# Optimization experiments

Hardware: AMD Instinct MI355X
Metric: run time of the kernel (lower is better)

The kernel has to match this reference:

```python
import jax, jax.numpy as jnp
import numpy as np
import math

B, N, DIM = 4, 4096, 1024
HEADS, DHEAD, NRF = 16, 64, 64
STAB = 1e-6  # numerical_stabilizer


def setup_inputs() -> dict:
    key = jax.random.key(0)
    k1, k2, k3, k4 = jax.random.split(key, 4)
    x = jax.random.normal(k1, (B, N, DIM), dtype=jnp.float32)
    W_qkv = jax.random.normal(k2, (DIM, 3 * HEADS * DHEAD), dtype=jnp.float32) * (1.0 / math.sqrt(DIM))
    RF = jax.random.normal(k3, (HEADS, DHEAD, NRF), dtype=jnp.float32) / math.sqrt(NRF)
    W_out = jax.random.normal(k4, (HEADS * DHEAD, DIM), dtype=jnp.float32) * (1.0 / math.sqrt(HEADS * DHEAD))
    b_out = jnp.zeros((DIM,), dtype=jnp.float32)
    return {"x": x, "W_qkv": W_qkv, "RF": RF, "W_out": W_out, "b_out": b_out}


def _phi(t, RF):
    # kernel transformation: project onto random features, then ReLU (default kernel)
    return jax.nn.relu(jnp.einsum('bhnd,hdr->bhnr', t, RF))


def reference(x, W_qkv, RF, W_out, b_out):
    b, n, _ = x.shape
    qkv = x @ W_qkv                                  # [b, n, 3*h*d]
    q, k, v = jnp.split(qkv, 3, axis=-1)
    def to_heads(t):
        return t.reshape(b, n, HEADS, DHEAD).transpose(0, 2, 1, 3)  # [b,h,n,d]
    q, k, v = to_heads(q), to_heads(k), to_heads(v)

    phi_q = _phi(q, RF)                              # [b,h,n,r]
    phi_k = _phi(k, RF)                              # [b,h,n,r]

    # linear-complexity FAVOR+ attention
    kv = jnp.einsum('bhnr,bhnd->bhrd', phi_k, v)     # [b,h,r,d]
    out = jnp.einsum('bhnr,bhrd->bhnd', phi_q, kv)   # [b,h,n,d]
    # normalizer: einsum('bhnr,bhmr->bhn') == phi_q @ sum_m(phi_k)
    k_sum = phi_k.sum(axis=2)                        # [b,h,r]
    normalizer = jnp.einsum('bhnr,bhr->bhn', phi_q, k_sum)[..., None] + STAB
    out = out / normalizer

    out = out.transpose(0, 2, 1, 3).reshape(b, n, HEADS * DHEAD)
    out = out @ W_out + b_out
    return out
```

## Files before the change

### kernel.cpp

```cpp
#include <hip/hip_runtime.h>


typedef __attribute__((ext_vector_type(8))) short s8v;
typedef __attribute__((ext_vector_type(4))) short s4v;
typedef __attribute__((ext_vector_type(4))) float f4v;
typedef __attribute__((ext_vector_type(4))) int   i4v;

#define MFMA16(a, b, c) __builtin_amdgcn_mfma_f32_16x16x32_bf16((a), (b), (c), 0, 0, 0)

__device__ __forceinline__ unsigned short f2bf(float f) {
  unsigned int u = __builtin_bit_cast(unsigned int, f);
  unsigned int r = (u + 0x7FFFu + ((u >> 16) & 1u)) >> 16;
  return (unsigned short)r;
}

__device__ __forceinline__ int swz(int p) {
  return p ^ (((p >> 7) & 7) << 4);
}

__device__ __forceinline__ void gl_lds16(const void* g, void* l) {
  __builtin_amdgcn_global_load_lds(
      (const __attribute__((address_space(1))) void*)g,
      (__attribute__((address_space(3))) void*)l, 16, 0, 0);
}

__global__ __launch_bounds__(256) void cvt_bf16(const float* __restrict__ in,
                                                unsigned short* __restrict__ out,
                                                int n4) {
  int i = blockIdx.x * 256 + threadIdx.x;
  if (i >= n4) return;
  f4v v = ((const f4v*)in)[i];
  s4v o;
#pragma unroll
  for (int j = 0; j < 4; ++j) o[j] = (short)f2bf(v[j]);
  ((s4v*)out)[i] = o;
}

__global__ __launch_bounds__(256) void transpose_cvt(const float* __restrict__ in,
                                                     unsigned short* __restrict__ out,
                                                     int R, int C) {
  __shared__ float tile[32][33];
  const int tx = threadIdx.x, ty = threadIdx.y;
  const int z = blockIdx.z;
  const float* inz = in + (size_t)z * R * C;
  unsigned short* outz = out + (size_t)z * R * C;
  const int c0 = blockIdx.x * 32, r0 = blockIdx.y * 32;
#pragma unroll
  for (int j = 0; j < 4; ++j)
    tile[ty + j * 8][tx] = inz[(size_t)(r0 + ty + j * 8) * C + c0 + tx];
  __syncthreads();
#pragma unroll
  for (int j = 0; j < 4; ++j)
    outz[(size_t)(c0 + ty + j * 8) * R + r0 + tx] = f2bf(tile[tx][ty + j * 8]);
}

template <int MODE>
__global__ __launch_bounds__(512, 2) void gemm256(const unsigned short* __restrict__ A,
                                                  const unsigned short* __restrict__ Bt,
                                                  void* __restrict__ Cout,
                                                  const float* __restrict__ bias,
                                                  int Nn, int K, int NTN, int CPX) {
  __shared__ __align__(128) unsigned short smem[65536];
  const int t = threadIdx.x, w = t >> 6, lane = t & 63;
  const int wm = w >> 2, wn = w & 3;
  const int fr = lane & 15, c16 = (lane >> 4) * 16;
  const int nkt = K >> 6;

  const int bid = blockIdx.x;
  const int wg = (bid & 7) * CPX + (bid >> 3);
  const int tm = wg / NTN, tn = wg % NTN;

  const unsigned short* gA = A + (size_t)tm * 256 * K;
  const unsigned short* gB = Bt + (size_t)tn * 256 * K;

  const int s0 = swz(t * 16);
  const int s1 = swz(8192 + t * 16);
  const int goff0 = (s0 >> 7) * K + ((s0 & 127) >> 1);
  const int goff1 = ((s1 - 8192) >> 7) * K + ((s1 & 127) >> 1) + 64 * K;
  const int woff = w * 1024;

  auto stage = [&](int T2, int part) {
    if (T2 >= nkt) return;
    char* reg = (char*)smem + (((T2 & 1) * 4 + part) << 14);
    const unsigned short* gp =
        (part < 2 ? gA : gB) + (size_t)((part & 1) * 128) * K + T2 * 64;
    gl_lds16(gp + goff0, reg + woff);
    gl_lds16(gp + goff1, reg + 8192 + woff);
  };

  f4v acc[8][4] = {};

  stage(0, 0); stage(0, 1); stage(0, 2); stage(0, 3);

  auto rdA = [&](int mh, s8v (&a)[4][2], const char* Ar) {
#pragma unroll
    for (int i = 0; i < 4; ++i)
#pragma unroll
      for (int ks = 0; ks < 2; ++ks) {
        int p = swz((mh * 64 + i * 16 + fr) * 128 + ks * 64 + c16);
        a[i][ks] = *(const s8v*)(Ar + p);
      }
  };
  auto rdB = [&](int nh, s8v (&b)[2][2], const char* Br, int brow) {
#pragma unroll
    for (int j = 0; j < 2; ++j)
#pragma unroll
      for (int ks = 0; ks < 2; ++ks) {
        int p = swz((brow + nh * 32 + j * 16 + fr) * 128 + ks * 64 + c16);
        b[j][ks] = *(const s8v*)(Br + p);
      }
  };
  auto mmac = [&](int mh, int nh, const s8v (&a)[4][2], const s8v (&b)[2][2]) {
    __builtin_amdgcn_s_setprio(1);
#pragma unroll
    for (int i = 0; i < 4; ++i)
#pragma unroll
      for (int j = 0; j < 2; ++j) {
        acc[mh * 4 + i][nh * 2 + j] = MFMA16(a[i][0], b[j][0], acc[mh * 4 + i][nh * 2 + j]);
        acc[mh * 4 + i][nh * 2 + j] = MFMA16(a[i][1], b[j][1], acc[mh * 4 + i][nh * 2 + j]);
      }
    __builtin_amdgcn_s_setprio(0);
  };

  const int brow = (wn & 1) * 64;
  for (int T = 0; T < nkt; ++T) {
    const int d = T & 1;
    const char* Ar = (const char*)smem + ((d * 4 + wm) << 14);
    const char* Br = (const char*)smem + ((d * 4 + 2 + (wn >> 1)) << 14);
    asm volatile("s_waitcnt vmcnt(0)" ::: "memory");
    __builtin_amdgcn_s_barrier();
    __builtin_amdgcn_sched_barrier(0);
    stage(T + 1, 0); stage(T + 1, 1); stage(T + 1, 2); stage(T + 1, 3);
    s8v a[4][2], b0[2][2], b1[2][2];
    rdA(0, a, Ar); rdB(0, b0, Br, brow); rdB(1, b1, Br, brow);
    mmac(0, 0, a, b0);
    mmac(0, 1, a, b1);
    rdA(1, a, Ar);
    mmac(1, 1, a, b1);
    mmac(1, 0, a, b0);
  }

#pragma unroll
  for (int m = 0; m < 8; ++m)
#pragma unroll
    for (int n = 0; n < 4; ++n) {
      const int row = tm * 256 + wm * 128 + m * 16 + (lane >> 4) * 4;
      const int col = tn * 256 + wn * 64 + n * 16 + fr;
      if (MODE == 0) {
        unsigned short* C = (unsigned short*)Cout;
#pragma unroll
        for (int r = 0; r < 4; ++r)
          C[(size_t)(row + r) * Nn + col] = f2bf(acc[m][n][r]);
      } else {
        float* C = (float*)Cout;
        const float bv = bias[col];
#pragma unroll
        for (int r = 0; r < 4; ++r)
          C[(size_t)(row + r) * Nn + col] = acc[m][n][r] + bv;
      }
    }
}

__global__ __launch_bounds__(256) void phik_kv(const unsigned short* __restrict__ qkv,
                                               const unsigned short* __restrict__ RFt,
                                               float* __restrict__ kvpart) {
  __shared__ unsigned short RFl[2 * 64 * 32];
  __shared__ unsigned short Kl[2 * 128 * 32];
  __shared__ unsigned short pht[64 * 136];
  __shared__ unsigned short vt[80 * 136];
  const int t = threadIdx.x, w = t >> 6, lane = t & 63;
  const int och = blockIdx.x, h = blockIdx.y, b = blockIdx.z;
  const int fr = lane & 15, kg = (lane >> 4) * 8;

#pragma unroll
  for (int i = 0; i < 2; ++i) {
    int unit = i * 256 + w * 64 + lane;
    int p = unit >> 8, rem = unit & 255;
    int r = rem >> 2, cg = (rem & 3) * 8;
    gl_lds16(RFt + ((h * 64 + r) * 64 + p * 32 + cg), &RFl[(i * 256 + w * 64) * 8]);
  }
  for (int i = t; i < 136; i += 256) vt[64 * 136 + i] = 0x3F80;
  for (int i = t; i < 15 * 136; i += 256) vt[65 * 136 + i] = 0;

  f4v kvacc[5] = {};

  for (int c = 0; c < 4; ++c) {
    const int n0c = och * 512 + c * 128;
    const size_t rowbase = (size_t)(b * 4096 + n0c);
#pragma unroll
    for (int i = 0; i < 4; ++i) {
      int unit = i * 256 + w * 64 + lane;
      int p = unit >> 9, rem = unit & 511;
      int n = rem >> 2, cg = (rem & 3) * 8;
      gl_lds16(qkv + (rowbase + n) * 3072 + 1024 + h * 64 + p * 32 + cg,
               &Kl[(i * 256 + w * 64) * 8]);
    }
    i4v vreg[4];
#pragma unroll
    for (int it = 0; it < 4; ++it) {
      int slot = it * 256 + t;
      vreg[it] = *(const i4v*)&qkv[(rowbase + (slot >> 3)) * 3072 + 2048 + h * 64 +
                                   (slot & 7) * 8];
    }
    __syncthreads();
    f4v pacc[2][4] = {};
#pragma unroll
    for (int p = 0; p < 2; ++p) {
      s8v ka[2], rb[4];
#pragma unroll
      for (int m = 0; m < 2; ++m)
        ka[m] = *(const s8v*)&Kl[p * 4096 + (w * 32 + m * 16 + fr) * 32 + kg];
#pragma unroll
      for (int rf = 0; rf < 4; ++rf)
        rb[rf] = *(const s8v*)&RFl[p * 2048 + (rf * 16 + fr) * 32 + kg];
#pragma unroll
      for (int m = 0; m < 2; ++m)
#pragma unroll
        for (int rf = 0; rf < 4; ++rf)
          pacc[m][rf] = MFMA16(ka[m], rb[rf], pacc[m][rf]);
    }
#pragma unroll
    for (int it = 0; it < 4; ++it) {
      int slot = it * 256 + t;
      int vn = slot >> 3, vdh = (slot & 7) * 8;
      const unsigned short* vr = (const unsigned short*)&vreg[it];
#pragma unroll
      for (int j = 0; j < 8; ++j) vt[(vdh + j) * 136 + vn] = vr[j];
    }
#pragma unroll
    for (int m = 0; m < 2; ++m)
#pragma unroll
      for (int rf = 0; rf < 4; ++rf) {
        int r = rf * 16 + fr;
        int nb = w * 32 + m * 16 + (lane >> 4) * 4;
        s4v pk;
#pragma unroll
        for (int g = 0; g < 4; ++g) pk[g] = (short)f2bf(fmaxf(pacc[m][rf][g], 0.0f));
        *(s4v*)&pht[r * 136 + nb] = pk;
      }
    __syncthreads();
#pragma unroll
    for (int kst = 0; kst < 4; ++kst) {
      s8v pb = *(const s8v*)&pht[(w * 16 + fr) * 136 + kst * 32 + kg];
#pragma unroll
      for (int f = 0; f < 5; ++f) {
        s8v va = *(const s8v*)&vt[(f * 16 + fr) * 136 + kst * 32 + kg];
        kvacc[f] = MFMA16(va, pb, kvacc[f]);
      }
    }
  }
  const int bh = b * 16 + h;
  float* outp = kvpart + ((size_t)bh * 8 + och) * (80 * 64);
#pragma unroll
  for (int f = 0; f < 5; ++f) {
    int row = f * 16 + (lane >> 4) * 4;
    int col = w * 16 + fr;
#pragma unroll
    for (int g = 0; g < 4; ++g) outp[(row + g) * 64 + col] = kvacc[f][g];
  }
}

__global__ __launch_bounds__(256) void kv_reduce(const float* __restrict__ kvpart,
                                                 unsigned short* __restrict__ kvt) {
  const int bh = blockIdx.x, t = threadIdx.x;
  for (int i = t; i < 80 * 64; i += 256) {
    float s = 0.f;
#pragma unroll
    for (int c = 0; c < 8; ++c) s += kvpart[((size_t)bh * 8 + c) * 5120 + i];
    kvt[(size_t)bh * 5120 + i] = f2bf(s);
  }
}

__global__ __launch_bounds__(256) void phiq_out(const unsigned short* __restrict__ qkv,
                                                const unsigned short* __restrict__ RFt,
                                                const unsigned short* __restrict__ kvt,
                                                unsigned short* __restrict__ attno) {
  __shared__ unsigned short RFl[2 * 64 * 32];
  __shared__ unsigned short Ql[2 * 128 * 32];
  __shared__ unsigned short phl[128 * 72];
  __shared__ unsigned short kvl[80 * 72];
  const int t = threadIdx.x, w = t >> 6, lane = t & 63;
  const int ch = blockIdx.x, h = blockIdx.y, b = blockIdx.z;
  const int fr = lane & 15, kg = (lane >> 4) * 8;
  const int bh = b * 16 + h;
  const size_t rowbase = (size_t)(b * 4096 + ch * 128);

#pragma unroll
  for (int i = 0; i < 2; ++i) {
    int unit = i * 256 + w * 64 + lane;
    int p = unit >> 8, rem = unit & 255;
    int r = rem >> 2, cg = (rem & 3) * 8;
    gl_lds16(RFt + ((h * 64 + r) * 64 + p * 32 + cg), &RFl[(i * 256 + w * 64) * 8]);
  }
#pragma unroll
  for (int i = 0; i < 4; ++i) {
    int unit = i * 256 + w * 64 + lane;
    int p = unit >> 9, rem = unit & 511;
    int n = rem >> 2, cg = (rem & 3) * 8;
    gl_lds16(qkv + (rowbase + n) * 3072 + h * 64 + p * 32 + cg,
             &Ql[(i * 256 + w * 64) * 8]);
  }
  for (int i = t; i < 640; i += 256) {
    int row = i >> 3, cg = (i & 7) * 8;
    *(i4v*)&kvl[row * 72 + cg] = *(const i4v*)&kvt[(size_t)bh * 5120 + row * 64 + cg];
  }
  __syncthreads();
  f4v pacc[2][4] = {};
#pragma unroll
  for (int p = 0; p < 2; ++p) {
    s8v qa[2], rb[4];
#pragma unroll
    for (int m = 0; m < 2; ++m)
      qa[m] = *(const s8v*)&Ql[p * 4096 + (w * 32 + m * 16 + fr) * 32 + kg];
#pragma unroll
    for (int rf = 0; rf < 4; ++rf)
      rb[rf] = *(const s8v*)&RFl[p * 2048 + (rf * 16 + fr) * 32 + kg];
#pragma unroll
    for (int m = 0; m < 2; ++m)
#pragma unroll
      for (int rf = 0; rf < 4; ++rf)
        pacc[m][rf] = MFMA16(qa[m], rb[rf], pacc[m][rf]);
  }
#pragma unroll
  for (int m = 0; m < 2; ++m)
#pragma unroll
    for (int rf = 0; rf < 4; ++rf) {
      int r = rf * 16 + fr;
      int nb = w * 32 + m * 16 + (lane >> 4) * 4;
#pragma unroll
      for (int g = 0; g < 4; ++g)
        phl[(nb + g) * 72 + r] = f2bf(fmaxf(pacc[m][rf][g], 0.0f));
    }
  __syncthreads();
  f4v acc[2][5] = {};
#pragma unroll
  for (int kst = 0; kst < 2; ++kst) {
    s8v pa[2], kb[5];
#pragma unroll
    for (int m = 0; m < 2; ++m)
      pa[m] = *(const s8v*)&phl[(w * 32 + m * 16 + fr) * 72 + kst * 32 + kg];
#pragma unroll
    for (int f = 0; f < 5; ++f)
      kb[f] = *(const s8v*)&kvl[(f * 16 + fr) * 72 + kst * 32 + kg];
#pragma unroll
    for (int m = 0; m < 2; ++m)
#pragma unroll
      for (int f = 0; f < 5; ++f) acc[m][f] = MFMA16(pa[m], kb[f], acc[m][f]);
  }
#pragma unroll
  for (int m = 0; m < 2; ++m)
#pragma unroll
    for (int g = 0; g < 4; ++g) {
      float nrm = __shfl(acc[m][4][g], lane & 48) + 1e-6f;
      int n = w * 32 + m * 16 + (lane >> 4) * 4 + g;
      size_t orow = rowbase + n;
#pragma unroll
      for (int f = 0; f < 4; ++f)
        attno[orow * 1024 + h * 64 + f * 16 + fr] = f2bf(acc[m][f][g] / nrm);
    }
}

extern "C" void kernel_launch(void* const* d_in, const int* in_sizes, int n_in,
                              void* d_out, int out_size, void* d_ws, size_t ws_size,
                              hipStream_t stream) {
  const float* x = (const float*)d_in[0];
  const float* W_qkv = (const float*)d_in[1];
  const float* RF = (const float*)d_in[2];
  const float* W_out = (const float*)d_in[3];
  const float* b_out = (const float*)d_in[4];
  float* out = (float*)d_out;

  char* ws = (char*)d_ws;
  size_t off = 0;
  auto alloc = [&](size_t bytes) -> void* {
    void* p = ws + off;
    off += (bytes + 255) & ~(size_t)255;
    return p;
  };
  unsigned short* xb = (unsigned short*)alloc(16384ull * 1024 * 2);
  unsigned short* wqkvt = (unsigned short*)alloc(3072ull * 1024 * 2);
  unsigned short* woutt = (unsigned short*)alloc(1024ull * 1024 * 2);
  unsigned short* rft = (unsigned short*)alloc(16ull * 64 * 64 * 2);
  unsigned short* qkv = (unsigned short*)alloc(16384ull * 3072 * 2);
  float* kvpart = (float*)alloc(64ull * 8 * 80 * 64 * 4);
  unsigned short* kvt = (unsigned short*)alloc(64ull * 80 * 64 * 2);
  unsigned short* attno = (unsigned short*)alloc(16384ull * 1024 * 2);

  cvt_bf16<<<16384, 256, 0, stream>>>(x, xb, 4194304);
  transpose_cvt<<<dim3(96, 32, 1), dim3(32, 8), 0, stream>>>(W_qkv, wqkvt, 1024, 3072);
  transpose_cvt<<<dim3(32, 32, 1), dim3(32, 8), 0, stream>>>(W_out, woutt, 1024, 1024);
  transpose_cvt<<<dim3(2, 2, 16), dim3(32, 8), 0, stream>>>(RF, rft, 64, 64);

  gemm256<0><<<768, 512, 0, stream>>>(xb, wqkvt, qkv, nullptr, 3072, 1024, 12, 96);
  phik_kv<<<dim3(8, 16, 4), 256, 0, stream>>>(qkv, rft, kvpart);
  kv_reduce<<<64, 256, 0, stream>>>(kvpart, kvt);
  phiq_out<<<dim3(32, 16, 4), 256, 0, stream>>>(qkv, rft, kvt, attno);
  gemm256<1><<<256, 512, 0, stream>>>(attno, woutt, out, b_out, 1024, 1024, 4, 32);
}
```

Before: 224.8 us.

## Fold random-feature projection into QKV weights and emit transposed phi_k and V

```diff
diff --git a/kernel.cpp b/kernel.cpp
--- a/kernel.cpp
+++ b/kernel.cpp
@@ -16,6 +16,9 @@
 
 __device__ __forceinline__ int swz(int p) {
   return p ^ (((p >> 7) & 7) << 4);
+}
+__device__ __forceinline__ int swz8(int p) {
+  return p ^ (((p >> 8) & 7) << 4);
 }
 
 __device__ __forceinline__ void gl_lds16(const void* g, void* l) {
@@ -41,23 +44,50 @@
                                                      int R, int C) {
   __shared__ float tile[32][33];
   const int tx = threadIdx.x, ty = threadIdx.y;
-  const int z = blockIdx.z;
-  const float* inz = in + (size_t)z * R * C;
-  unsigned short* outz = out + (size_t)z * R * C;
   const int c0 = blockIdx.x * 32, r0 = blockIdx.y * 32;
 #pragma unroll
   for (int j = 0; j < 4; ++j)
-    tile[ty + j * 8][tx] = inz[(size_t)(r0 + ty + j * 8) * C + c0 + tx];
+    tile[ty + j * 8][tx] = in[(size_t)(r0 + ty + j * 8) * C + c0 + tx];
   __syncthreads();
 #pragma unroll
   for (int j = 0; j < 4; ++j)
-    outz[(size_t)(c0 + ty + j * 8) * R + r0 + tx] = f2bf(tile[tx][ty + j * 8]);
+    out[(size_t)(c0 + ty + j * 8) * R + r0 + tx] = f2bf(tile[tx][ty + j * 8]);
+}
+
+__global__ __launch_bounds__(256) void fold_w(const float* __restrict__ W_qkv,
+                                              const float* __restrict__ RF,
+                                              unsigned short* __restrict__ wqkvt) {
+  __shared__ float RFl[64 * 64];
+  __shared__ float Wl[128 * 65];
+  const int t = threadIdx.x;
+  const int k0 = blockIdx.x * 128, h = blockIdx.y, part = blockIdx.z;
+#pragma unroll
+  for (int i = 0; i < 16; ++i) RFl[i * 256 + t] = RF[h * 4096 + i * 256 + t];
+#pragma unroll
+  for (int i = 0; i < 32; ++i) {
+    int idx = i * 256 + t, kk = idx >> 6, d = idx & 63;
+    Wl[kk * 65 + d] = W_qkv[(size_t)(k0 + kk) * 3072 + part * 1024 + h * 64 + d];
+  }
+  __syncthreads();
+  const int w = t >> 6, lane = t & 63;
+  const int rg = w >> 1;
+  const int kk = (w & 1) * 64 + lane;
+#pragma unroll
+  for (int j = 0; j < 32; ++j) {
+    const int r = rg * 32 + j;
+    float s = 0.f;
+#pragma unroll
+    for (int d = 0; d < 64; ++d) s += Wl[kk * 65 + d] * RFl[d * 64 + r];
+    wqkvt[(size_t)(part * 1024 + h * 64 + r) * 1024 + k0 + kk] = f2bf(s);
+  }
 }
 
 template <int MODE>
 __global__ __launch_bounds__(512, 2) void gemm256(const unsigned short* __restrict__ A,
                                                   const unsigned short* __restrict__ Bt,
                                                   void* __restrict__ Cout,
+                                                  unsigned short* __restrict__ kT,
+                                                  unsigned short* __restrict__ vT,
                                                   const float* __restrict__ bias,
                                                   int Nn, int K, int NTN, int CPX) {
   __shared__ __align__(128) unsigned short smem[65536];
@@ -89,7 +119,6 @@
   };
 
   f4v acc[8][4] = {};
-
   stage(0, 0); stage(0, 1); stage(0, 2); stage(0, 3);
 
   auto rdA = [&](int mh, s8v (&a)[4][2], const char* Ar) {
@@ -140,6 +169,7 @@
     mmac(1, 0, a, b0);
   }
 
+  const int sec = tn >> 2;
 #pragma unroll
   for (int m = 0; m < 8; ++m)
 #pragma unroll
@@ -147,10 +177,21 @@
       const int row = tm * 256 + wm * 128 + m * 16 + (lane >> 4) * 4;
       const int col = tn * 256 + wn * 64 + n * 16 + fr;
       if (MODE == 0) {
-        unsigned short* C = (unsigned short*)Cout;
-#pragma unroll
-        for (int r = 0; r < 4; ++r)
-          C[(size_t)(row + r) * Nn + col] = f2bf(acc[m][n][r]);
+        if (sec == 0) {
+          unsigned short* C = (unsigned short*)Cout;
+#pragma unroll
+          for (int r = 0; r < 4; ++r)
+            C[(size_t)(row + r) * 1024 + col] = f2bf(fmaxf(acc[m][n][r], 0.0f));
+        } else {
+          const int cl = col & 1023;
+          const int bh = (row >> 12) * 16 + (cl >> 6);
+          unsigned short* T = (sec == 1) ? kT : vT;
+          s4v o;
+#pragma unroll
+          for (int g = 0; g < 4; ++g)
+            o[g] = (short)f2bf(sec == 1 ? fmaxf(acc[m][n][g], 0.0f) : acc[m][n][g]);
+          *(s4v*)&T[((size_t)bh * 64 + (cl & 63)) * 4096 + (row & 4095)] = o;
+        }
       } else {
         float* C = (float*)Cout;
         const float bv = bias[col];
@@ -161,103 +202,67 @@
     }
 }
 
-__global__ __launch_bounds__(256) void phik_kv(const unsigned short* __restrict__ qkv,
-                                               const unsigned short* __restrict__ RFt,
+__global__ __launch_bounds__(256) void kv_gemm(const unsigned short* __restrict__ kT,
+                                               const unsigned short* __restrict__ vT,
                                                float* __restrict__ kvpart) {
-  __shared__ unsigned short RFl[2 * 64 * 32];
-  __shared__ unsigned short Kl[2 * 128 * 32];
-  __shared__ unsigned short pht[64 * 136];
-  __shared__ unsigned short vt[80 * 136];
+  __shared__ __align__(128) char lds[2 * 36864];
   const int t = threadIdx.x, w = t >> 6, lane = t & 63;
-  const int och = blockIdx.x, h = blockIdx.y, b = blockIdx.z;
-  const int fr = lane & 15, kg = (lane >> 4) * 8;
-
-#pragma unroll
-  for (int i = 0; i < 2; ++i) {
-    int unit = i * 256 + w * 64 + lane;
-    int p = unit >> 8, rem = unit & 255;
-    int r = rem >> 2, cg = (rem & 3) * 8;
-    gl_lds16(RFt + ((h * 64 + r) * 64 + p * 32 + cg), &RFl[(i * 256 + w * 64) * 8]);
-  }
-  for (int i = t; i < 136; i += 256) vt[64 * 136 + i] = 0x3F80;
-  for (int i = t; i < 15 * 136; i += 256) vt[65 * 136 + i] = 0;
+  const int och = blockIdx.x, bh = blockIdx.y;
+  const int fr = lane & 15, c16 = (lane >> 4) * 16;
+  const char* kTb = (const char*)kT + (size_t)bh * 64 * 8192 + och * 1024;
+  const char* vTb = (const char*)vT + (size_t)bh * 64 * 8192 + och * 1024;
+
+  for (int i = t; i < 2 * 2048; i += 256) {
+    int buf = i >> 11, e = i & 2047;
+    int row = 64 + (e >> 7), c = e & 127;
+    int p = swz8(row * 256 + c * 2);
+    *(unsigned short*)&lds[buf * 36864 + 16384 + p] = (row == 64) ? 0x3F80 : 0;
+  }
+
+  int srcoff[4];
+#pragma unroll
+  for (int i = 0; i < 4; ++i) {
+    int p = swz8((i * 256 + t) * 16);
+    srcoff[i] = (p >> 8) * 8192 + (p & 255);
+  }
+  auto stage = [&](int s) {
+    if (s >= 4) return;
+    char* base = lds + (s & 1) * 36864;
+#pragma unroll
+    for (int i = 0; i < 4; ++i) {
+      gl_lds16(kTb + s * 256 + srcoff[i], base + (i * 256 + w * 64) * 16);
+      gl_lds16(vTb + s * 256 + srcoff[i], base + 16384 + (i * 256 + w * 64) * 16);
+    }
+  };
 
   f4v kvacc[5] = {};
-
-  for (int c = 0; c < 4; ++c) {
-    const int n0c = och * 512 + c * 128;
-    const size_t rowbase = (size_t)(b * 4096 + n0c);
-#pragma unroll
-    for (int i = 0; i < 4; ++i) {
-      int unit = i * 256 + w * 64 + lane;
-      int p = unit >> 9, rem = unit & 511;
-      int n = rem >> 2, cg = (rem & 3) * 8;
-      gl_lds16(qkv + (rowbase + n) * 3072 + 1024 + h * 64 + p * 32 + cg,
-               &Kl[(i * 256 + w * 64) * 8]);
+  stage(0);
+  for (int s = 0; s < 4; ++s) {
+    asm volatile("s_waitcnt vmcnt(0)" ::: "memory");
+    __builtin_amdgcn_s_barrier();
+    __builtin_amdgcn_sched_barrier(0);
+    stage(s + 1);
+    const char* kB = lds + (s & 1) * 36864;
+    const char* vB = kB + 16384;
+    s8v a[4];
+#pragma unroll
+    for (int ks = 0; ks < 4; ++ks)
+      a[ks] = *(const s8v*)(kB + swz8((w * 16 + fr) * 256 + ks * 64 + c16));
+    __builtin_amdgcn_s_setprio(1);
+#pragma unroll
+    for (int f = 0; f < 5; ++f) {
+#pragma unroll
+      for (int ks = 0; ks < 4; ++ks) {
+        s8v b = *(const s8v*)(vB + swz8((f * 16 + fr) * 256 + ks * 64 + c16));
+        kvacc[f] = MFMA16(a[ks], b, kvacc[f]);
+      }
     }
-    i4v vreg[4];
-#pragma unroll
-    for (int it = 0; it < 4; ++it) {
-      int slot = it * 256 + t;
-      vreg[it] = *(const i4v*)&qkv[(rowbase + (slot >> 3)) * 3072 + 2048 + h * 64 +
-                                   (slot & 7) * 8];
-    }
-    __syncthreads();
-    f4v pacc[2][4] = {};
-#pragma unroll
-    for (int p = 0; p < 2; ++p) {
-      s8v ka[2], rb[4];
-#pragma unroll
-      for (int m = 0; m < 2; ++m)
-        ka[m] = *(const s8v*)&Kl[p * 4096 + (w * 32 + m * 16 + fr) * 32 + kg];
-#pragma unroll
-      for (int rf = 0; rf < 4; ++rf)
-        rb[rf] = *(const s8v*)&RFl[p * 2048 + (rf * 16 + fr) * 32 + kg];
-#pragma unroll
-      for (int m = 0; m < 2; ++m)
-#pragma unroll
-        for (int rf = 0; rf < 4; ++rf)
-          pacc[m][rf] = MFMA16(ka[m], rb[rf], pacc[m][rf]);
-    }
-#pragma unroll
-    for (int it = 0; it < 4; ++it) {
-      int slot = it * 256 + t;
-      int vn = slot >> 3, vdh = (slot & 7) * 8;
-      const unsigned short* vr = (const unsigned short*)&vreg[it];
-#pragma unroll
-      for (int j = 0; j < 8; ++j) vt[(vdh + j) * 136 + vn] = vr[j];
-    }
-#pragma unroll
-    for (int m = 0; m < 2; ++m)
-#pragma unroll
-      for (int rf = 0; rf < 4; ++rf) {
-        int r = rf * 16 + fr;
-        int nb = w * 32 + m * 16 + (lane >> 4) * 4;
-        s4v pk;
-#pragma unroll
-        for (int g = 0; g < 4; ++g) pk[g] = (short)f2bf(fmaxf(pacc[m][rf][g], 0.0f));
-        *(s4v*)&pht[r * 136 + nb] = pk;
-      }
-    __syncthreads();
-#pragma unroll
-    for (int kst = 0; kst < 4; ++kst) {
-      s8v pb = *(const s8v*)&pht[(w * 16 + fr) * 136 + kst * 32 + kg];
-#pragma unroll
-      for (int f = 0; f < 5; ++f) {
-        s8v va = *(const s8v*)&vt[(f * 16 + fr) * 136 + kst * 32 + kg];
-        kvacc[f] = MFMA16(va, pb, kvacc[f]);
-      }
-    }
-  }
-  const int bh = b * 16 + h;
+    __builtin_amdgcn_s_setprio(0);
+  }
   float* outp = kvpart + ((size_t)bh * 8 + och) * (80 * 64);
 #pragma unroll
-  for (int f = 0; f < 5; ++f) {
-    int row = f * 16 + (lane >> 4) * 4;
-    int col = w * 16 + fr;
-#pragma unroll
-    for (int g = 0; g < 4; ++g) outp[(row + g) * 64 + col] = kvacc[f][g];
-  }
+  for (int f = 0; f < 5; ++f)
+    *(f4v*)&outp[(f * 16 + fr) * 64 + w * 16 + (lane >> 4) * 4] = kvacc[f];
 }
 
 __global__ __launch_bounds__(256) void kv_reduce(const float* __restrict__ kvpart,
@@ -271,77 +276,41 @@
   }
 }
 
-__global__ __launch_bounds__(256) void phiq_out(const unsigned short* __restrict__ qkv,
-                                                const unsigned short* __restrict__ RFt,
+__global__ __launch_bounds__(256) void phiq_out(const unsigned short* __restrict__ phiq,
                                                 const unsigned short* __restrict__ kvt,
                                                 unsigned short* __restrict__ attno) {
-  __shared__ unsigned short RFl[2 * 64 * 32];
-  __shared__ unsigned short Ql[2 * 128 * 32];
-  __shared__ unsigned short phl[128 * 72];
+  __shared__ __align__(128) unsigned short phl[128 * 64];
   __shared__ unsigned short kvl[80 * 72];
   const int t = threadIdx.x, w = t >> 6, lane = t & 63;
   const int ch = blockIdx.x, h = blockIdx.y, b = blockIdx.z;
-  const int fr = lane & 15, kg = (lane >> 4) * 8;
+  const int fr = lane & 15, kg = (lane >> 4) * 8, c16 = (lane >> 4) * 16;
   const int bh = b * 16 + h;
   const size_t rowbase = (size_t)(b * 4096 + ch * 128);
-
-#pragma unroll
-  for (int i = 0; i < 2; ++i) {
-    int unit = i * 256 + w * 64 + lane;
-    int p = unit >> 8, rem = unit & 255;
-    int r = rem >> 2, cg = (rem & 3) * 8;
-    gl_lds16(RFt + ((h * 64 + r) * 64 + p * 32 + cg), &RFl[(i * 256 + w * 64) * 8]);
-  }
+  const char* src = (const char*)phiq + rowbase * 2048 + h * 128;
+
 #pragma unroll
   for (int i = 0; i < 4; ++i) {
-    int unit = i * 256 + w * 64 + lane;
-    int p = unit >> 9, rem = unit & 511;
-    int n = rem >> 2, cg = (rem & 3) * 8;
-    gl_lds16(qkv + (rowbase + n) * 3072 + h * 64 + p * 32 + cg,
-             &Ql[(i * 256 + w * 64) * 8]);
+    int p = swz((i * 256 + t) * 16);
+    gl_lds16(src + (p >> 7) * 2048 + (p & 127),
+             (char*)phl + (i * 256 + w * 64) * 16);
   }
   for (int i = t; i < 640; i += 256) {
     int row = i >> 3, cg = (i & 7) * 8;
     *(i4v*)&kvl[row * 72 + cg] = *(const i4v*)&kvt[(size_t)bh * 5120 + row * 64 + cg];
   }
   __syncthreads();
-  f4v pacc[2][4] = {};
-#pragma unroll
-  for (int p = 0; p < 2; ++p) {
-    s8v qa[2], rb[4];
+
+  f4v acc[2][5] = {};
+#pragma unroll
+  for (int ks = 0; ks < 2; ++ks) {
+    s8v pa[2], kb[5];
 #pragma unroll
     for (int m = 0; m < 2; ++m)
-      qa[m] = *(const s8v*)&Ql[p * 4096 + (w * 32 + m * 16 + fr) * 32 + kg];
-#pragma unroll
-    for (int rf = 0; rf < 4; ++rf)
-      rb[rf] = *(const s8v*)&RFl[p * 2048 + (rf * 16 + fr) * 32 + kg];
-#pragma unroll
-    for (int m = 0; m < 2; ++m)
-#pragma unroll
-      for (int rf = 0; rf < 4; ++rf)
-        pacc[m][rf] = MFMA16(qa[m], rb[rf], pacc[m][rf]);
-  }
-#pragma unroll
-  for (int m = 0; m < 2; ++m)
-#pragma unroll
-    for (int rf = 0; rf < 4; ++rf) {
-      int r = rf * 16 + fr;
-      int nb = w * 32 + m * 16 + (lane >> 4) * 4;
-#pragma unroll
-      for (int g = 0; g < 4; ++g)
-        phl[(nb + g) * 72 + r] = f2bf(fmaxf(pacc[m][rf][g], 0.0f));
-    }
-  __syncthreads();
-  f4v acc[2][5] = {};
-#pragma unroll
-  for (int kst = 0; kst < 2; ++kst) {
-    s8v pa[2], kb[5];
-#pragma unroll
-    for (int m = 0; m < 2; ++m)
-      pa[m] = *(const s8v*)&phl[(w * 32 + m * 16 + fr) * 72 + kst * 32 + kg];
+      pa[m] = *(const s8v*)((const char*)phl +
+                            swz((w * 32 + m * 16 + fr) * 128 + ks * 64 + c16));
 #pragma unroll
     for (int f = 0; f < 5; ++f)
-      kb[f] = *(const s8v*)&kvl[(f * 16 + fr) * 72 + kst * 32 + kg];
+      kb[f] = *(const s8v*)&kvl[(f * 16 + fr) * 72 + ks * 32 + kg];
 #pragma unroll
     for (int m = 0; m < 2; ++m)
 #pragma unroll
@@ -380,20 +349,23 @@
   unsigned short* xb = (unsigned short*)alloc(16384ull * 1024 * 2);
   unsigned short* wqkvt = (unsigned short*)alloc(3072ull * 1024 * 2);
   unsigned short* woutt = (unsigned short*)alloc(1024ull * 1024 * 2);
-  unsigned short* rft = (unsigned short*)alloc(16ull * 64 * 64 * 2);
-  unsigned short* qkv = (unsigned short*)alloc(16384ull * 3072 * 2);
+  unsigned short* phiq = (unsigned short*)alloc(16384ull * 1024 * 2);
+  unsigned short* kT = (unsigned short*)alloc(64ull * 64 * 4096 * 2);
+  unsigned short* vT = (unsigned short*)alloc(64ull * 64 * 4096 * 2);
   float* kvpart = (float*)alloc(64ull * 8 * 80 * 64 * 4);
   unsigned short* kvt = (unsigned short*)alloc(64ull * 80 * 64 * 2);
   unsigned short* attno = (unsigned short*)alloc(16384ull * 1024 * 2);
 
   cvt_bf16<<<16384, 256, 0, stream>>>(x, xb, 4194304);
-  transpose_cvt<<<dim3(96, 32, 1), dim3(32, 8), 0, stream>>>(W_qkv, wqkvt, 1024, 3072);
-  transpose_cvt<<<dim3(32, 32, 1), dim3(32, 8), 0, stream>>>(W_out, woutt, 1024, 1024);
-  transpose_cvt<<<dim3(2, 2, 16), dim3(32, 8), 0, stream>>>(RF, rft, 64, 64);
-
-  gemm256<0><<<768, 512, 0, stream>>>(xb, wqkvt, qkv, nullptr, 3072, 1024, 12, 96);
-  phik_kv<<<dim3(8, 16, 4), 256, 0, stream>>>(qkv, rft, kvpart);
+  transpose_cvt<<<dim3(96, 32), dim3(32, 8), 0, stream>>>(W_qkv, wqkvt, 1024, 3072);
+  transpose_cvt<<<dim3(32, 32), dim3(32, 8), 0, stream>>>(W_out, woutt, 1024, 1024);
+  fold_w<<<dim3(8, 16, 2), 256, 0, stream>>>(W_qkv, RF, wqkvt);
+
+  gemm256<0><<<768, 512, 0, stream>>>(xb, wqkvt, phiq, kT, vT, nullptr,
+                                      3072, 1024, 12, 96);
+  kv_gemm<<<dim3(8, 64), 256, 0, stream>>>(kT, vT, kvpart);
   kv_reduce<<<64, 256, 0, stream>>>(kvpart, kvt);
-  phiq_out<<<dim3(32, 16, 4), 256, 0, stream>>>(qkv, rft, kvt, attno);
-  gemm256<1><<<256, 512, 0, stream>>>(attno, woutt, out, b_out, 1024, 1024, 4, 32);
-}
+  phiq_out<<<dim3(32, 16, 4), 256, 0, stream>>>(phiq, kvt, attno);
+  gemm256<1><<<256, 512, 0, stream>>>(attno, woutt, out, nullptr, nullptr, b_out,
+                                      1024, 1024, 4, 32);
+}
```

Result: slower. 260.4 us (+15.9%).
